# Kernel optimization log

Hardware: AMD Instinct MI355X
Metric: run time of the kernel (lower is better)

The kernel has to match this reference:

```python
import jax, jax.numpy as jnp
import numpy as np

B, N, C = 8, 4096, 512
K = 512   # key_channels
V = 512   # value_channels (must equal in_channels for reprojection to typecheck)
H = 8     # head_count


def setup_inputs() -> dict:
    key = jax.random.key(0)
    ks = jax.random.split(key, 10)
    s = 1.0 / np.sqrt(C)
    return {
        "input_": jax.random.normal(ks[0], (B, N, C), jnp.float32),
        "y": jax.random.normal(ks[1], (B, N, C), jnp.float32),
        "Wk": jax.random.uniform(ks[2], (C, K), jnp.float32, -s, s),
        "bk": jax.random.uniform(ks[3], (K,), jnp.float32, -s, s),
        "Wq": jax.random.uniform(ks[4], (C, K), jnp.float32, -s, s),
        "bq": jax.random.uniform(ks[5], (K,), jnp.float32, -s, s),
        "Wv": jax.random.uniform(ks[6], (C, K), jnp.float32, -s, s),
        "bv": jax.random.uniform(ks[7], (K,), jnp.float32, -s, s),
        "Wr": jax.random.uniform(ks[8], (C, K), jnp.float32, -s, s),
        "br": jax.random.uniform(ks[9], (K,), jnp.float32, -s, s),
    }


def reference(input_, y, Wk, bk, Wq, bq, Wv, bv, Wr, br):
    hk = K // H  # head key channels
    hv = V // H  # head value channels
    # projections -> [B, N, H, h]
    keys = ((input_ + y) @ Wk + bk).reshape(B, N, H, hk)
    queries = (y @ Wq + bq).reshape(B, N, H, hk)
    values = (input_ @ Wv + bv).reshape(B, N, H, hv)
    # key softmax over tokens N; query softmax over head channels hk
    keys = jax.nn.softmax(keys, axis=1)
    queries = jax.nn.softmax(queries, axis=3)
    # context[b,h,k,v] = sum_n key[b,n,h,k] * value[b,n,h,v]
    context = jnp.einsum('bnhk,bnhv->bhkv', keys, values)
    # attended[b,n,h,v] = sum_k context[b,h,k,v] * query[b,n,h,k]
    attended = jnp.einsum('bhkv,bnhk->bnhv', context, queries)
    aggregated = attended.reshape(B, N, V)  # concat heads over value channels
    return aggregated @ Wr + br
```

## Files before the change

### kernel.cpp

```cpp
#include <hip/hip_runtime.h>
#include <hip/hip_bf16.h>
#include <stdint.h>


typedef __attribute__((ext_vector_type(8))) short short8;
typedef __attribute__((ext_vector_type(4))) float f32x4;
typedef __attribute__((ext_vector_type(4))) unsigned short us4;

__device__ __forceinline__ unsigned short f2bf(float f) {
  union { float f; unsigned u; } v; v.f = f;
  unsigned r = v.u + 0x7FFFu + ((v.u >> 16) & 1u);
  return (unsigned short)(r >> 16);
}
__device__ __forceinline__ float bf2f(unsigned short u) {
  union { unsigned u; float f; } v; v.u = ((unsigned)u) << 16;
  return v.f;
}
__device__ __forceinline__ ushort2 pk2(float a, float b) {
  __hip_bfloat162 h = __float22bfloat162_rn(float2{a, b});
  return *reinterpret_cast<ushort2*>(&h);
}
__device__ __forceinline__ void gload16(const void* g, void* l) {
  __builtin_amdgcn_global_load_lds(
      (const __attribute__((address_space(1))) void*)g,
      (__attribute__((address_space(3))) void*)l, 16, 0, 0);
}

__global__ void prep_w(const float* __restrict__ Wk, const float* __restrict__ Wq,
                       const float* __restrict__ Wv, const float* __restrict__ Wr,
                       unsigned short* __restrict__ Wt) {
  __shared__ float tile[64][65];
  const int t = threadIdx.x;
  const int bx = blockIdx.x, by = blockIdx.y, w = blockIdx.z;
  const float* W = (w == 0) ? Wk : (w == 1) ? Wq : (w == 2) ? Wv : Wr;
  unsigned short* O = Wt + (size_t)w * 512 * 512;
#pragma unroll
  for (int p = 0; p < 16; ++p) {
    int idx = p * 256 + t; int r = idx >> 6, c = idx & 63;
    tile[r][c] = W[(size_t)(by * 64 + r) * 512 + bx * 64 + c];
  }
  __syncthreads();
#pragma unroll
  for (int p = 0; p < 16; ++p) {
    int idx = p * 256 + t; int r = idx >> 6, c = idx & 63;
    O[(size_t)(bx * 64 + r) * 512 + by * 64 + c] = f2bf(tile[c][r]);
  }
}

__global__ __launch_bounds__(256) void prep_xy(const float* __restrict__ x, const float* __restrict__ y,
                        unsigned short* __restrict__ xb, unsigned short* __restrict__ yb,
                        unsigned short* __restrict__ xyb) {
  const size_t total = (size_t)8 * 4096 * 512;
  const size_t stride = (size_t)gridDim.x * 256 * 16;
  for (size_t i0 = ((size_t)blockIdx.x * 256 + threadIdx.x) * 16; i0 < total; i0 += stride) {
    float4 a[4], b[4];
#pragma unroll
    for (int q = 0; q < 4; ++q) { a[q] = *(const float4*)(x + i0 + q * 4); }
#pragma unroll
    for (int q = 0; q < 4; ++q) { b[q] = *(const float4*)(y + i0 + q * 4); }
#pragma unroll
    for (int h = 0; h < 2; ++h) {
      float4 a0 = a[2 * h], a1 = a[2 * h + 1], b0 = b[2 * h], b1 = b[2 * h + 1];
      short8 vx, vy, vs;
      ushort2 p;
      p = pk2(a0.x, a0.y); vx[0] = (short)p.x; vx[1] = (short)p.y;
      p = pk2(a0.z, a0.w); vx[2] = (short)p.x; vx[3] = (short)p.y;
      p = pk2(a1.x, a1.y); vx[4] = (short)p.x; vx[5] = (short)p.y;
      p = pk2(a1.z, a1.w); vx[6] = (short)p.x; vx[7] = (short)p.y;
      p = pk2(b0.x, b0.y); vy[0] = (short)p.x; vy[1] = (short)p.y;
      p = pk2(b0.z, b0.w); vy[2] = (short)p.x; vy[3] = (short)p.y;
      p = pk2(b1.x, b1.y); vy[4] = (short)p.x; vy[5] = (short)p.y;
      p = pk2(b1.z, b1.w); vy[6] = (short)p.x; vy[7] = (short)p.y;
      p = pk2(a0.x + b0.x, a0.y + b0.y); vs[0] = (short)p.x; vs[1] = (short)p.y;
      p = pk2(a0.z + b0.z, a0.w + b0.w); vs[2] = (short)p.x; vs[3] = (short)p.y;
      p = pk2(a1.x + b1.x, a1.y + b1.y); vs[4] = (short)p.x; vs[5] = (short)p.y;
      p = pk2(a1.z + b1.z, a1.w + b1.w); vs[6] = (short)p.x; vs[7] = (short)p.y;
      *(short8*)(xb + i0 + h * 8) = vx;
      *(short8*)(yb + i0 + h * 8) = vy;
      *(short8*)(xyb + i0 + h * 8) = vs;
    }
  }
}

template <int MODE>
__global__ __launch_bounds__(256) void gemm_bf16(const unsigned short* __restrict__ A,
                          const unsigned short* __restrict__ Bmat,
                          const float* __restrict__ bias, void* __restrict__ OutV) {
  __shared__ __align__(16) unsigned short As[2][128][64];
  __shared__ __align__(16) unsigned short Bs[2][128][64];
  const int t = threadIdx.x, l = t & 63, w = t >> 6;
  const int lr = l & 15, lg = l >> 4;
  const int wr = w >> 1, wc = w & 1;
  const int bid = blockIdx.x;
  const int swz = (bid & 7) * 128 + (bid >> 3);
  const int tn = swz & 3, tm = swz >> 2;

  const unsigned short* Bbase = (MODE == 3) ? (Bmat + (size_t)(tm >> 5) * 262144) : Bmat;
  const int r0 = w * 8 + (l >> 3);
  const int su = ((l & 7) ^ (l >> 3)) * 8;
  const unsigned short* Ag = A + (size_t)(tm * 128 + r0) * 512 + su;
  const unsigned short* Bg = Bbase + (size_t)(tn * 128 + r0) * 512 + su;

  f32x4 acc[4][4] = {};

#define PSTAGE(buf, kt)                                                        \
  {                                                                            \
    _Pragma("unroll") for (int i = 0; i < 4; ++i) {                            \
      gload16(Ag + (size_t)i * 32 * 512 + (kt) * 64, &As[buf][i * 32 + w * 8][0]); \
      gload16(Bg + (size_t)i * 32 * 512 + (kt) * 64, &Bs[buf][i * 32 + w * 8][0]); \
    }                                                                          \
  }

  PSTAGE(0, 0)
  PSTAGE(1, 1)
  for (int kt = 0; kt < 8; ++kt) {
    const int cur = kt & 1;
    if (kt < 7) { asm volatile("s_waitcnt vmcnt(8)" ::: "memory"); }
    else        { asm volatile("s_waitcnt vmcnt(0)" ::: "memory"); }
    __builtin_amdgcn_s_barrier();
    asm volatile("" ::: "memory");
    __builtin_amdgcn_s_setprio(1);
#pragma unroll
    for (int kk = 0; kk < 2; ++kk) {
      short8 af[4], bf[4];
#pragma unroll
      for (int m = 0; m < 4; ++m)
        af[m] = *(const short8*)&As[cur][wr * 64 + m * 16 + lr][((kk * 4 + lg) ^ (lr & 7)) * 8];
#pragma unroll
      for (int n = 0; n < 4; ++n)
        bf[n] = *(const short8*)&Bs[cur][wc * 64 + n * 16 + lr][((kk * 4 + lg) ^ (lr & 7)) * 8];
#pragma unroll
      for (int m = 0; m < 4; ++m)
#pragma unroll
        for (int n = 0; n < 4; ++n)
          acc[m][n] = __builtin_amdgcn_mfma_f32_16x16x32_bf16(af[m], bf[n], acc[m][n], 0, 0, 0);
    }
    __builtin_amdgcn_s_setprio(0);
    asm volatile("" ::: "memory");
    __builtin_amdgcn_s_barrier();
    asm volatile("" ::: "memory");
    if (kt < 6) PSTAGE(cur, kt + 2)
  }
#undef PSTAGE

  const int c_base = tn * 128 + wc * 64;
  const int r_base = tm * 128 + wr * 64;
  float bv_[4];
#pragma unroll
  for (int n = 0; n < 4; ++n) bv_[n] = bias[c_base + n * 16 + lr];

  if (MODE == 1) {
    unsigned short* Out = (unsigned short*)OutV;
#pragma unroll
    for (int m = 0; m < 4; ++m) {
#pragma unroll
      for (int j = 0; j < 4; ++j) {
        float a0 = acc[m][0][j] + bv_[0], a1 = acc[m][1][j] + bv_[1];
        float a2 = acc[m][2][j] + bv_[2], a3 = acc[m][3][j] + bv_[3];
        float mx = fmaxf(fmaxf(a0, a1), fmaxf(a2, a3));
#pragma unroll
        for (int o = 1; o < 16; o <<= 1) mx = fmaxf(mx, __shfl_xor(mx, o));
        float e0 = __expf(a0 - mx), e1 = __expf(a1 - mx);
        float e2 = __expf(a2 - mx), e3 = __expf(a3 - mx);
        float s = e0 + e1 + e2 + e3;
#pragma unroll
        for (int o = 1; o < 16; o <<= 1) s += __shfl_xor(s, o);
        const float rs = 1.0f / s;
        const int row = r_base + m * 16 + lg * 4 + j;
        Out[(size_t)row * 512 + c_base + 0 * 16 + lr] = f2bf(e0 * rs);
        Out[(size_t)row * 512 + c_base + 1 * 16 + lr] = f2bf(e1 * rs);
        Out[(size_t)row * 512 + c_base + 2 * 16 + lr] = f2bf(e2 * rs);
        Out[(size_t)row * 512 + c_base + 3 * 16 + lr] = f2bf(e3 * rs);
      }
    }
  } else if (MODE == 3) {
    float* Out = (float*)OutV;
#pragma unroll
    for (int n = 0; n < 4; ++n) {
      const int col = c_base + n * 16 + lr;
#pragma unroll
      for (int m = 0; m < 4; ++m) {
        const int row = r_base + m * 16 + lg * 4;
#pragma unroll
        for (int j = 0; j < 4; ++j)
          Out[(size_t)(row + j) * 512 + col] = acc[m][n][j] + bv_[n];
      }
    }
  } else {
    unsigned short* Out = (unsigned short*)OutV;
#pragma unroll
    for (int n = 0; n < 4; ++n) {
      const int col = c_base + n * 16 + lr;
#pragma unroll
      for (int m = 0; m < 4; ++m) {
        const int row = r_base + m * 16 + lg * 4;
        const int b = row >> 12, nl = row & 4095;
        us4 v;
#pragma unroll
        for (int j = 0; j < 4; ++j) {
          float f = acc[m][n][j] + bv_[n];
          if (MODE == 0) f = __expf(f);
          v[j] = f2bf(f);
        }
        *(us4*)&Out[((size_t)(b * 512 + col)) * 4096 + nl] = v;
      }
    }
  }
}

__global__ void ssum(const unsigned short* __restrict__ KeT, float* __restrict__ S) {
  const int t = threadIdx.x;
  const int row = blockIdx.x;
  const unsigned short* p = KeT + (size_t)row * 4096 + t * 16;
  float s = 0.f;
#pragma unroll
  for (int q = 0; q < 2; ++q) {
    short8 v = *(const short8*)(p + q * 8);
#pragma unroll
    for (int j = 0; j < 8; ++j) s += bf2f((unsigned short)v[j]);
  }
#pragma unroll
  for (int o = 32; o; o >>= 1) s += __shfl_xor(s, o);
  __shared__ float ls[4];
  if ((t & 63) == 0) ls[t >> 6] = s;
  __syncthreads();
  if (t == 0) S[row] = ls[0] + ls[1] + ls[2] + ls[3];
}

__global__ void context_partial(const unsigned short* __restrict__ KeT,
                                const unsigned short* __restrict__ VT,
                                float* __restrict__ cp) {
  const int t = threadIdx.x, l = t & 63, w = t >> 6;
  const int lr = l & 15, lg = l >> 4;
  const int ch = blockIdx.x, h = blockIdx.y, b = blockIdx.z;
  const unsigned short* Kp = KeT + ((size_t)b * 512 + h * 64) * 4096;
  const unsigned short* Vp = VT + ((size_t)b * 512 + h * 64) * 4096;
  const int tok_w = ch * 1024 + w * 256;
  f32x4 acc[4][4] = {};
  for (int s = 0; s < 8; ++s) {
    const int tok = tok_w + s * 32 + lg * 8;
    short8 a[4], kf[4];
#pragma unroll
    for (int m = 0; m < 4; ++m) a[m] = *(const short8*)&Vp[(size_t)(m * 16 + lr) * 4096 + tok];
#pragma unroll
    for (int n = 0; n < 4; ++n) kf[n] = *(const short8*)&Kp[(size_t)(n * 16 + lr) * 4096 + tok];
#pragma unroll
    for (int m = 0; m < 4; ++m)
#pragma unroll
      for (int n = 0; n < 4; ++n)
        acc[m][n] = __builtin_amdgcn_mfma_f32_16x16x32_bf16(a[m], kf[n], acc[m][n], 0, 0, 0);
  }
  __shared__ float red[4][64][64];
#pragma unroll
  for (int m = 0; m < 4; ++m)
#pragma unroll
    for (int n = 0; n < 4; ++n)
#pragma unroll
      for (int j = 0; j < 4; ++j)
        red[w][m * 16 + lg * 4 + j][n * 16 + lr] = acc[m][n][j];
  __syncthreads();
  const int blk = (b * 8 + h) * 4 + ch;
  float* o = cp + (size_t)blk * 4096;
  for (int i = 0; i < 16; ++i) {
    int e = i * 256 + t;
    int v = e >> 6, k = e & 63;
    o[e] = red[0][v][k] + red[1][v][k] + red[2][v][k] + red[3][v][k];
  }
}

__global__ void ctx_reduce(const float* __restrict__ cp, const float* __restrict__ S,
                           unsigned short* __restrict__ ctxN) {
  const int bh = blockIdx.x, t = threadIdx.x;
  const float* p = cp + (size_t)bh * 4 * 4096;
  for (int i = 0; i < 16; ++i) {
    int e = i * 256 + t;
    float vsum = p[e] + p[4096 + e] + p[8192 + e] + p[12288 + e];
    int v = e >> 6, k = e & 63;
    ctxN[(size_t)bh * 4096 + k * 64 + v] = f2bf(vsum / S[bh * 64 + k]);
  }
}

__global__ void ctx_mm(const unsigned short* __restrict__ ctxN, const unsigned short* __restrict__ Wrt,
                       unsigned short* __restrict__ MT) {
  const int t = threadIdx.x, l = t & 63, w = t >> 6;
  const int lr = l & 15, lg = l >> 4;
  const int h = blockIdx.x, b = blockIdx.y;
  const unsigned short* Ap = ctxN + (size_t)(b * 8 + h) * 4096;
  f32x4 acc[4][8] = {};
  const int c0 = w * 128;
#pragma unroll
  for (int kk = 0; kk < 2; ++kk) {
    const int vb = kk * 32 + lg * 8;
    short8 a[4], bfr[8];
#pragma unroll
    for (int m = 0; m < 4; ++m) a[m] = *(const short8*)&Ap[(m * 16 + lr) * 64 + vb];
#pragma unroll
    for (int n = 0; n < 8; ++n) bfr[n] = *(const short8*)&Wrt[(size_t)(c0 + n * 16 + lr) * 512 + h * 64 + vb];
#pragma unroll
    for (int m = 0; m < 4; ++m)
#pragma unroll
      for (int n = 0; n < 8; ++n)
        acc[m][n] = __builtin_amdgcn_mfma_f32_16x16x32_bf16(a[m], bfr[n], acc[m][n], 0, 0, 0);
  }
#pragma unroll
  for (int n = 0; n < 8; ++n) {
    const int c = c0 + n * 16 + lr;
#pragma unroll
    for (int m = 0; m < 4; ++m) {
      const int k = m * 16 + lg * 4;
      us4 v;
#pragma unroll
      for (int j = 0; j < 4; ++j) v[j] = f2bf(acc[m][n][j]);
      *(us4*)&MT[((size_t)b * 512 + c) * 512 + h * 64 + k] = v;
    }
  }
}

extern "C" void kernel_launch(void* const* d_in, const int* in_sizes, int n_in,
                              void* d_out, int out_size, void* d_ws, size_t ws_size,
                              hipStream_t stream) {
  (void)in_sizes; (void)n_in; (void)out_size; (void)ws_size;
  const float* x  = (const float*)d_in[0];
  const float* y  = (const float*)d_in[1];
  const float* Wk = (const float*)d_in[2];
  const float* bk = (const float*)d_in[3];
  const float* Wq = (const float*)d_in[4];
  const float* bq = (const float*)d_in[5];
  const float* Wv = (const float*)d_in[6];
  const float* bv = (const float*)d_in[7];
  const float* Wr = (const float*)d_in[8];
  const float* br = (const float*)d_in[9];
  float* out = (float*)d_out;

  char* ws = (char*)d_ws;
  unsigned short* Wt   = (unsigned short*)(ws + 0);
  unsigned short* xb   = (unsigned short*)(ws + 2097152);
  unsigned short* yb   = (unsigned short*)(ws + 35651584);
  unsigned short* xyb  = (unsigned short*)(ws + 69206016);
  unsigned short* KeT  = (unsigned short*)(ws + 102760448);
  unsigned short* VT   = (unsigned short*)(ws + 136314880);
  float* S             = (float*)(ws + 169869312);
  float* cp            = (float*)(ws + 169885696);
  unsigned short* ctxN = (unsigned short*)(ws + 174080000);
  unsigned short* MT   = (unsigned short*)(ws + 174604288);
  unsigned short* Qp   = xyb;

  prep_w<<<dim3(8, 8, 4), 256, 0, stream>>>(Wk, Wq, Wv, Wr, Wt);
  prep_xy<<<2048, 256, 0, stream>>>(x, y, xb, yb, xyb);
  gemm_bf16<0><<<1024, 256, 0, stream>>>(xyb, Wt, bk, KeT);
  ssum<<<4096, 256, 0, stream>>>(KeT, S);
  gemm_bf16<2><<<1024, 256, 0, stream>>>(xb, Wt + 2 * 262144, bv, VT);
  gemm_bf16<1><<<1024, 256, 0, stream>>>(yb, Wt + 262144, bq, Qp);
  context_partial<<<dim3(4, 8, 8), 256, 0, stream>>>(KeT, VT, cp);
  ctx_reduce<<<64, 256, 0, stream>>>(cp, S, ctxN);
  ctx_mm<<<dim3(8, 8), 256, 0, stream>>>(ctxN, Wt + 3 * 262144, MT);
  gemm_bf16<3><<<1024, 256, 0, stream>>>(Qp, MT, br, out);
}
```

Measured before the change: 214.8 us.

## Merge three projection GEMMs into one launch and fuse key-sum via atomics

The K, V and Q projection GEMMs now run as sections of a single 3072-block launch, dispatched by block index, when the workspace has room for a separate Q buffer. The per-row key exponential sums are accumulated in the GEMM epilogue with shuffle reductions and atomicAdd, which removes the separate ssum kernel that re-read KeT. prep_xy drops its grid-stride loop, and the final GEMM becomes its own kernel. In exchange the change adds atomics, a memset, and branches on section inside the GEMM.

Result: slower. 223.5 us (+4.0%).

```diff
diff --git a/kernel.cpp b/kernel.cpp
--- a/kernel.cpp
+++ b/kernel.cpp
@@ -50,52 +50,55 @@
 __global__ __launch_bounds__(256) void prep_xy(const float* __restrict__ x, const float* __restrict__ y,
                         unsigned short* __restrict__ xb, unsigned short* __restrict__ yb,
                         unsigned short* __restrict__ xyb) {
-  const size_t total = (size_t)8 * 4096 * 512;
-  const size_t stride = (size_t)gridDim.x * 256 * 16;
-  for (size_t i0 = ((size_t)blockIdx.x * 256 + threadIdx.x) * 16; i0 < total; i0 += stride) {
-    float4 a[4], b[4];
-#pragma unroll
-    for (int q = 0; q < 4; ++q) { a[q] = *(const float4*)(x + i0 + q * 4); }
-#pragma unroll
-    for (int q = 0; q < 4; ++q) { b[q] = *(const float4*)(y + i0 + q * 4); }
-#pragma unroll
-    for (int h = 0; h < 2; ++h) {
-      float4 a0 = a[2 * h], a1 = a[2 * h + 1], b0 = b[2 * h], b1 = b[2 * h + 1];
-      short8 vx, vy, vs;
-      ushort2 p;
-      p = pk2(a0.x, a0.y); vx[0] = (short)p.x; vx[1] = (short)p.y;
-      p = pk2(a0.z, a0.w); vx[2] = (short)p.x; vx[3] = (short)p.y;
-      p = pk2(a1.x, a1.y); vx[4] = (short)p.x; vx[5] = (short)p.y;
-      p = pk2(a1.z, a1.w); vx[6] = (short)p.x; vx[7] = (short)p.y;
-      p = pk2(b0.x, b0.y); vy[0] = (short)p.x; vy[1] = (short)p.y;
-      p = pk2(b0.z, b0.w); vy[2] = (short)p.x; vy[3] = (short)p.y;
-      p = pk2(b1.x, b1.y); vy[4] = (short)p.x; vy[5] = (short)p.y;
-      p = pk2(b1.z, b1.w); vy[6] = (short)p.x; vy[7] = (short)p.y;
-      p = pk2(a0.x + b0.x, a0.y + b0.y); vs[0] = (short)p.x; vs[1] = (short)p.y;
-      p = pk2(a0.z + b0.z, a0.w + b0.w); vs[2] = (short)p.x; vs[3] = (short)p.y;
-      p = pk2(a1.x + b1.x, a1.y + b1.y); vs[4] = (short)p.x; vs[5] = (short)p.y;
-      p = pk2(a1.z + b1.z, a1.w + b1.w); vs[6] = (short)p.x; vs[7] = (short)p.y;
-      *(short8*)(xb + i0 + h * 8) = vx;
-      *(short8*)(yb + i0 + h * 8) = vy;
-      *(short8*)(xyb + i0 + h * 8) = vs;
-    }
-  }
-}
-
-template <int MODE>
-__global__ __launch_bounds__(256) void gemm_bf16(const unsigned short* __restrict__ A,
-                          const unsigned short* __restrict__ Bmat,
-                          const float* __restrict__ bias, void* __restrict__ OutV) {
+  const size_t i = ((size_t)blockIdx.x * 256 + threadIdx.x) * 16;
+  float4 a[4], b[4];
+#pragma unroll
+  for (int q = 0; q < 4; ++q) a[q] = *(const float4*)(x + i + q * 4);
+#pragma unroll
+  for (int q = 0; q < 4; ++q) b[q] = *(const float4*)(y + i + q * 4);
+#pragma unroll
+  for (int h = 0; h < 2; ++h) {
+    float4 a0 = a[2 * h], a1 = a[2 * h + 1], b0 = b[2 * h], b1 = b[2 * h + 1];
+    short8 vx, vy, vs;
+    ushort2 p;
+    p = pk2(a0.x, a0.y); vx[0] = (short)p.x; vx[1] = (short)p.y;
+    p = pk2(a0.z, a0.w); vx[2] = (short)p.x; vx[3] = (short)p.y;
+    p = pk2(a1.x, a1.y); vx[4] = (short)p.x; vx[5] = (short)p.y;
+    p = pk2(a1.z, a1.w); vx[6] = (short)p.x; vx[7] = (short)p.y;
+    p = pk2(b0.x, b0.y); vy[0] = (short)p.x; vy[1] = (short)p.y;
+    p = pk2(b0.z, b0.w); vy[2] = (short)p.x; vy[3] = (short)p.y;
+    p = pk2(b1.x, b1.y); vy[4] = (short)p.x; vy[5] = (short)p.y;
+    p = pk2(b1.z, b1.w); vy[6] = (short)p.x; vy[7] = (short)p.y;
+    p = pk2(a0.x + b0.x, a0.y + b0.y); vs[0] = (short)p.x; vs[1] = (short)p.y;
+    p = pk2(a0.z + b0.z, a0.w + b0.w); vs[2] = (short)p.x; vs[3] = (short)p.y;
+    p = pk2(a1.x + b1.x, a1.y + b1.y); vs[4] = (short)p.x; vs[5] = (short)p.y;
+    p = pk2(a1.z + b1.z, a1.w + b1.w); vs[6] = (short)p.x; vs[7] = (short)p.y;
+    *(short8*)(xb + i + h * 8) = vx;
+    *(short8*)(yb + i + h * 8) = vy;
+    *(short8*)(xyb + i + h * 8) = vs;
+  }
+}
+
+__global__ __launch_bounds__(256) void gemm_proj3(
+    const unsigned short* __restrict__ xyb, const unsigned short* __restrict__ xb,
+    const unsigned short* __restrict__ yb, const unsigned short* __restrict__ Wt,
+    const float* __restrict__ bk, const float* __restrict__ bv, const float* __restrict__ bq,
+    unsigned short* __restrict__ KeT, unsigned short* __restrict__ VT,
+    unsigned short* __restrict__ Qp, float* __restrict__ S, int sec_off) {
   __shared__ __align__(16) unsigned short As[2][128][64];
   __shared__ __align__(16) unsigned short Bs[2][128][64];
   const int t = threadIdx.x, l = t & 63, w = t >> 6;
   const int lr = l & 15, lg = l >> 4;
   const int wr = w >> 1, wc = w & 1;
-  const int bid = blockIdx.x;
+  const int sec = (int)(blockIdx.x >> 10) + sec_off;
+  const int bid = blockIdx.x & 1023;
   const int swz = (bid & 7) * 128 + (bid >> 3);
   const int tn = swz & 3, tm = swz >> 2;
 
-  const unsigned short* Bbase = (MODE == 3) ? (Bmat + (size_t)(tm >> 5) * 262144) : Bmat;
+  const unsigned short* A = (sec == 0) ? xyb : (sec == 1) ? xb : yb;
+  const unsigned short* Bbase = Wt + (size_t)((sec == 0) ? 0 : (sec == 1) ? 2 : 1) * 262144;
+  const float* bias = (sec == 0) ? bk : (sec == 1) ? bv : bq;
+
   const int r0 = w * 8 + (l >> 3);
   const int su = ((l & 7) ^ (l >> 3)) * 8;
   const unsigned short* Ag = A + (size_t)(tm * 128 + r0) * 512 + su;
@@ -149,8 +152,7 @@
 #pragma unroll
   for (int n = 0; n < 4; ++n) bv_[n] = bias[c_base + n * 16 + lr];
 
-  if (MODE == 1) {
-    unsigned short* Out = (unsigned short*)OutV;
+  if (sec == 2) {
 #pragma unroll
     for (int m = 0; m < 4; ++m) {
 #pragma unroll
@@ -167,64 +169,51 @@
         for (int o = 1; o < 16; o <<= 1) s += __shfl_xor(s, o);
         const float rs = 1.0f / s;
         const int row = r_base + m * 16 + lg * 4 + j;
-        Out[(size_t)row * 512 + c_base + 0 * 16 + lr] = f2bf(e0 * rs);
-        Out[(size_t)row * 512 + c_base + 1 * 16 + lr] = f2bf(e1 * rs);
-        Out[(size_t)row * 512 + c_base + 2 * 16 + lr] = f2bf(e2 * rs);
-        Out[(size_t)row * 512 + c_base + 3 * 16 + lr] = f2bf(e3 * rs);
+        Qp[(size_t)row * 512 + c_base + 0 * 16 + lr] = f2bf(e0 * rs);
+        Qp[(size_t)row * 512 + c_base + 1 * 16 + lr] = f2bf(e1 * rs);
+        Qp[(size_t)row * 512 + c_base + 2 * 16 + lr] = f2bf(e2 * rs);
+        Qp[(size_t)row * 512 + c_base + 3 * 16 + lr] = f2bf(e3 * rs);
       }
     }
-  } else if (MODE == 3) {
-    float* Out = (float*)OutV;
+  } else if (sec == 0) {
+    const int b = (tm * 128) >> 12;
 #pragma unroll
     for (int n = 0; n < 4; ++n) {
       const int col = c_base + n * 16 + lr;
+      float srow = 0.f;
 #pragma unroll
       for (int m = 0; m < 4; ++m) {
         const int row = r_base + m * 16 + lg * 4;
-#pragma unroll
-        for (int j = 0; j < 4; ++j)
-          Out[(size_t)(row + j) * 512 + col] = acc[m][n][j] + bv_[n];
+        const int nl = row & 4095;
+        us4 v;
+#pragma unroll
+        for (int j = 0; j < 4; ++j) {
+          float f = __expf(acc[m][n][j] + bv_[n]);
+          srow += f;
+          v[j] = f2bf(f);
+        }
+        *(us4*)&KeT[((size_t)(b * 512 + col)) * 4096 + nl] = v;
       }
+      srow += __shfl_xor(srow, 16);
+      srow += __shfl_xor(srow, 32);
+      if (lg == 0) atomicAdd(&S[b * 512 + col], srow);
     }
   } else {
-    unsigned short* Out = (unsigned short*)OutV;
+    const int b = (tm * 128) >> 12;
 #pragma unroll
     for (int n = 0; n < 4; ++n) {
       const int col = c_base + n * 16 + lr;
 #pragma unroll
       for (int m = 0; m < 4; ++m) {
         const int row = r_base + m * 16 + lg * 4;
-        const int b = row >> 12, nl = row & 4095;
+        const int nl = row & 4095;
         us4 v;
 #pragma unroll
-        for (int j = 0; j < 4; ++j) {
-          float f = acc[m][n][j] + bv_[n];
-          if (MODE == 0) f = __expf(f);
-          v[j] = f2bf(f);
-        }
-        *(us4*)&Out[((size_t)(b * 512 + col)) * 4096 + nl] = v;
+        for (int j = 0; j < 4; ++j) v[j] = f2bf(acc[m][n][j] + bv_[n]);
+        *(us4*)&VT[((size_t)(b * 512 + col)) * 4096 + nl] = v;
       }
     }
   }
-}
-
-__global__ void ssum(const unsigned short* __restrict__ KeT, float* __restrict__ S) {
-  const int t = threadIdx.x;
-  const int row = blockIdx.x;
-  const unsigned short* p = KeT + (size_t)row * 4096 + t * 16;
-  float s = 0.f;
-#pragma unroll
-  for (int q = 0; q < 2; ++q) {
-    short8 v = *(const short8*)(p + q * 8);
-#pragma unroll
-    for (int j = 0; j < 8; ++j) s += bf2f((unsigned short)v[j]);
-  }
-#pragma unroll
-  for (int o = 32; o; o >>= 1) s += __shfl_xor(s, o);
-  __shared__ float ls[4];
-  if ((t & 63) == 0) ls[t >> 6] = s;
-  __syncthreads();
-  if (t == 0) S[row] = ls[0] + ls[1] + ls[2] + ls[3];
 }
 
 __global__ void context_partial(const unsigned short* __restrict__ KeT,
@@ -316,10 +305,86 @@
   }
 }
 
+__global__ __launch_bounds__(256) void gemm_final(const unsigned short* __restrict__ Qs,
+                           const unsigned short* __restrict__ MT,
+                           const float* __restrict__ br, float* __restrict__ out) {
+  __shared__ __align__(16) unsigned short As[2][128][64];
+  __shared__ __align__(16) unsigned short Bs[2][128][64];
+  const int t = threadIdx.x, l = t & 63, w = t >> 6;
+  const int lr = l & 15, lg = l >> 4;
+  const int wr = w >> 1, wc = w & 1;
+  const int bid = blockIdx.x;
+  const int swz = (bid & 7) * 128 + (bid >> 3);
+  const int tn = swz & 3, tm = swz >> 2;
+
+  const unsigned short* Bbase = MT + (size_t)(tm >> 5) * 262144;
+  const int r0 = w * 8 + (l >> 3);
+  const int su = ((l & 7) ^ (l >> 3)) * 8;
+  const unsigned short* Ag = Qs + (size_t)(tm * 128 + r0) * 512 + su;
+  const unsigned short* Bg = Bbase + (size_t)(tn * 128 + r0) * 512 + su;
+
+  f32x4 acc[4][4] = {};
+
+#define PSTAGE(buf, kt)                                                        \
+  {                                                                            \
+    _Pragma("unroll") for (int i = 0; i < 4; ++i) {                            \
+      gload16(Ag + (size_t)i * 32 * 512 + (kt) * 64, &As[buf][i * 32 + w * 8][0]); \
+      gload16(Bg + (size_t)i * 32 * 512 + (kt) * 64, &Bs[buf][i * 32 + w * 8][0]); \
+    }                                                                          \
+  }
+
+  PSTAGE(0, 0)
+  PSTAGE(1, 1)
+  for (int kt = 0; kt < 8; ++kt) {
+    const int cur = kt & 1;
+    if (kt < 7) { asm volatile("s_waitcnt vmcnt(8)" ::: "memory"); }
+    else        { asm volatile("s_waitcnt vmcnt(0)" ::: "memory"); }
+    __builtin_amdgcn_s_barrier();
+    asm volatile("" ::: "memory");
+    __builtin_amdgcn_s_setprio(1);
+#pragma unroll
+    for (int kk = 0; kk < 2; ++kk) {
+      short8 af[4], bf[4];
+#pragma unroll
+      for (int m = 0; m < 4; ++m)
+        af[m] = *(const short8*)&As[cur][wr * 64 + m * 16 + lr][((kk * 4 + lg) ^ (lr & 7)) * 8];
+#pragma unroll
+      for (int n = 0; n < 4; ++n)
+        bf[n] = *(const short8*)&Bs[cur][wc * 64 + n * 16 + lr][((kk * 4 + lg) ^ (lr & 7)) * 8];
+#pragma unroll
+      for (int m = 0; m < 4; ++m)
+#pragma unroll
+        for (int n = 0; n < 4; ++n)
+          acc[m][n] = __builtin_amdgcn_mfma_f32_16x16x32_bf16(af[m], bf[n], acc[m][n], 0, 0, 0);
+    }
+    __builtin_amdgcn_s_setprio(0);
+    asm volatile("" ::: "memory");
+    __builtin_amdgcn_s_barrier();
+    asm volatile("" ::: "memory");
+    if (kt < 6) PSTAGE(cur, kt + 2)
+  }
+#undef PSTAGE
+
+  const int c_base = tn * 128 + wc * 64;
+  const int r_base = tm * 128 + wr * 64;
+#pragma unroll
+  for (int n = 0; n < 4; ++n) {
+    const int col = c_base + n * 16 + lr;
+    const float bs = br[col];
+#pragma unroll
+    for (int m = 0; m < 4; ++m) {
+      const int row = r_base + m * 16 + lg * 4;
+#pragma unroll
+      for (int j = 0; j < 4; ++j)
+        out[(size_t)(row + j) * 512 + col] = acc[m][n][j] + bs;
+    }
+  }
+}
+
 extern "C" void kernel_launch(void* const* d_in, const int* in_sizes, int n_in,
                               void* d_out, int out_size, void* d_ws, size_t ws_size,
                               hipStream_t stream) {
-  (void)in_sizes; (void)n_in; (void)out_size; (void)ws_size;
+  (void)in_sizes; (void)n_in; (void)out_size;
   const float* x  = (const float*)d_in[0];
   const float* y  = (const float*)d_in[1];
   const float* Wk = (const float*)d_in[2];
@@ -343,16 +408,21 @@
   float* cp            = (float*)(ws + 169885696);
   unsigned short* ctxN = (unsigned short*)(ws + 174080000);
   unsigned short* MT   = (unsigned short*)(ws + 174604288);
-  unsigned short* Qp   = xyb;
+  unsigned short* QpX  = (unsigned short*)(ws + 178798592);
+  const bool wide = ws_size >= (size_t)210364416;
+  unsigned short* Qp   = wide ? QpX : xyb;
 
   prep_w<<<dim3(8, 8, 4), 256, 0, stream>>>(Wk, Wq, Wv, Wr, Wt);
-  prep_xy<<<2048, 256, 0, stream>>>(x, y, xb, yb, xyb);
-  gemm_bf16<0><<<1024, 256, 0, stream>>>(xyb, Wt, bk, KeT);
-  ssum<<<4096, 256, 0, stream>>>(KeT, S);
-  gemm_bf16<2><<<1024, 256, 0, stream>>>(xb, Wt + 2 * 262144, bv, VT);
-  gemm_bf16<1><<<1024, 256, 0, stream>>>(yb, Wt + 262144, bq, Qp);
+  prep_xy<<<4096, 256, 0, stream>>>(x, y, xb, yb, xyb);
+  hipMemsetAsync(S, 0, 512 * 8 * sizeof(float), stream);
+  if (wide) {
+    gemm_proj3<<<3072, 256, 0, stream>>>(xyb, xb, yb, Wt, bk, bv, bq, KeT, VT, Qp, S, 0);
+  } else {
+    gemm_proj3<<<2048, 256, 0, stream>>>(xyb, xb, yb, Wt, bk, bv, bq, KeT, VT, Qp, S, 0);
+    gemm_proj3<<<1024, 256, 0, stream>>>(xyb, xb, yb, Wt, bk, bv, bq, KeT, VT, Qp, S, 2);
+  }
   context_partial<<<dim3(4, 8, 8), 256, 0, stream>>>(KeT, VT, cp);
   ctx_reduce<<<64, 256, 0, stream>>>(cp, S, ctxN);
   ctx_mm<<<dim3(8, 8), 256, 0, stream>>>(ctxN, Wt + 3 * 262144, MT);
-  gemm_bf16<3><<<1024, 256, 0, stream>>>(Qp, MT, br, out);
-}
+  gemm_final<<<1024, 256, 0, stream>>>(Qp, MT, br, out);
+}
```
